# Kernel optimization log

Hardware: AMD Instinct MI355X
Metric: run time of the kernel (lower is better)

Reference implementation:

```python
import jax, jax.numpy as jnp
import numpy as np

B, S, D, H, DFF, N_LAYERS, BLK = 4, 1024, 1024, 16, 4096, 4, 64
DH = D // H
LN_EPS = 1e-5


def setup_inputs() -> dict:
    key = jax.random.key(0)
    ks = jax.random.split(key, 13)
    s = 0.02
    L = N_LAYERS
    return {
        "x": jax.random.normal(ks[0], (B, S, D), jnp.float32),
        "in_proj_w": jax.random.normal(ks[1], (L, 3 * D, D), jnp.float32) * s,
        "in_proj_b": jnp.zeros((L, 3 * D), jnp.float32),
        "out_w": jax.random.normal(ks[2], (L, D, D), jnp.float32) * s,
        "out_b": jnp.zeros((L, D), jnp.float32),
        "ln1_w": jnp.ones((L, D), jnp.float32),
        "ln1_b": jnp.zeros((L, D), jnp.float32),
        "lin1_w": jax.random.normal(ks[3], (L, DFF, D), jnp.float32) * s,
        "lin1_b": jnp.zeros((L, DFF), jnp.float32),
        "lin2_w": jax.random.normal(ks[4], (L, D, DFF), jnp.float32) * s,
        "lin2_b": jnp.zeros((L, D), jnp.float32),
        "ln2_w": jnp.ones((L, D), jnp.float32),
        "ln2_b": jnp.zeros((L, D), jnp.float32),
    }


def _layer_norm(x, w, b):
    mu = jnp.mean(x, axis=-1, keepdims=True)
    var = jnp.mean(jnp.square(x - mu), axis=-1, keepdims=True)
    return (x - mu) * jax.lax.rsqrt(var + LN_EPS) * w + b


def _forward(x, in_proj_w, in_proj_b, out_w, out_b, ln1_w, ln1_b,
             lin1_w, lin1_b, lin2_w, lin2_b, ln2_w, ln2_b):
    # block-causal additive bias: token may attend to current and previous blocks
    blk = jnp.arange(S) // BLK
    bias = jnp.where(blk[:, None] >= blk[None, :], 0.0, -jnp.inf)  # [S,S]
    scale = 1.0 / np.sqrt(DH).astype(np.float32)

    for l in range(N_LAYERS):
        # --- self-attention (post-norm, PyTorch TransformerEncoderLayer default) ---
        qkv = x @ in_proj_w[l].T + in_proj_b[l]            # [B,S,3D]
        q, k, v = jnp.split(qkv, 3, axis=-1)
        q = q.reshape(B, S, H, DH).transpose(0, 2, 1, 3)   # [B,H,S,DH]
        k = k.reshape(B, S, H, DH).transpose(0, 2, 1, 3)
        v = v.reshape(B, S, H, DH).transpose(0, 2, 1, 3)
        scores = jnp.einsum('bhqd,bhkd->bhqk', q, k) * scale + bias
        attn = jax.nn.softmax(scores, axis=-1)
        o = jnp.einsum('bhqk,bhkd->bhqd', attn, v)
        o = o.transpose(0, 2, 1, 3).reshape(B, S, D)
        o = o @ out_w[l].T + out_b[l]
        x = _layer_norm(x + o, ln1_w[l], ln1_b[l])
        # --- feed-forward (relu) ---
        h = jax.nn.relu(x @ lin1_w[l].T + lin1_b[l]) @ lin2_w[l].T + lin2_b[l]
        x = _layer_norm(x + h, ln2_w[l], ln2_b[l])
    return x


def reference(x, in_proj_w, in_proj_b, out_w, out_b, ln1_w, ln1_b,
              lin1_w, lin1_b, lin2_w, lin2_b, ln2_w, ln2_b):
    return _forward(x, in_proj_w, in_proj_b, out_w, out_b, ln1_w, ln1_b,
                    lin1_w, lin1_b, lin2_w, lin2_b, ln2_w, ln2_b)
```

## Files before the change

### kernel.cpp

```cpp
#include <hip/hip_runtime.h>
#include <stdint.h>

typedef __bf16 bf16;
typedef __bf16 bf16x8 __attribute__((ext_vector_type(8)));
typedef __bf16 bf16x4 __attribute__((ext_vector_type(4)));
typedef float  f32x4  __attribute__((ext_vector_type(4)));

#define B_   4
#define S_   1024
#define D_   1024
#define H_   16
#define DH_  64
#define DFF_ 4096
#define NL_  4
#define M_   (B_*S_)

__device__ __forceinline__ void async_copy16(const void* g, void* l) {
  __builtin_amdgcn_global_load_lds(
      (const __attribute__((address_space(1))) char*)(uintptr_t)g,
      (__attribute__((address_space(3))) char*)(uintptr_t)l,
      16, 0, 0);
}

template<int RELU, int MODE, int QKV, int BK>
__global__ __launch_bounds__(256) void gemm_bt_kernel(
    const bf16* __restrict__ A,
    const bf16* __restrict__ W,
    const float* __restrict__ bias,
    float* __restrict__ Cf,
    bf16*  __restrict__ Cb,
    bf16*  __restrict__ VtOut,
    int N, int Ktot, int Kc, int gx, int PN, int PM, int bpk)
{
  constexpr int NI = (BK == 64) ? 4 : 2;
  __shared__ bf16 As[2][128*BK];
  __shared__ bf16 Bs[2][128*BK];

  const int tid  = threadIdx.x;
  const int wave = tid >> 6;
  const int lane = tid & 63;
  const int wr = wave >> 1, wc = wave & 1;
  const int q4  = lane >> 4;
  const int l15 = lane & 15;

  const int Lg  = blockIdx.x;
  const int kz  = Lg / bpk;
  const int L   = Lg % bpk;
  const int xcd = L & 7;
  const int s   = L >> 3;
  const int Gn  = gx / PN;
  const int bn = ((xcd % Gn)*PN + (s % PN)) << 7;
  const int bm = ((xcd / Gn)*PM + (s / PN)) << 7;
  const int kstart = kz * Kc;

  const bf16* agp[NI]; const bf16* wgp[NI];
  int ldsb[NI];
  if constexpr (BK == 64) {
    const int r_loc = lane >> 3, c8 = lane & 7;
#pragma unroll
    for (int j = 0; j < NI; ++j) {
      const int rr = wave*32 + j*8 + r_loc;
      const int ko = ((c8 ^ (rr & 7)) << 3);
      agp[j] = A + (size_t)(bm + rr)*Ktot + kstart + ko;
      wgp[j] = W + (size_t)(bn + rr)*Ktot + kstart + ko;
      ldsb[j] = (wave*32 + j*8) * 64;
    }
  } else {
    const int r_loc = lane >> 2, c4 = lane & 3;
#pragma unroll
    for (int j = 0; j < NI; ++j) {
      const int rr = wave*32 + j*16 + r_loc;
      const int ko = ((c4 ^ ((rr >> 1) & 3)) << 3);
      agp[j] = A + (size_t)(bm + rr)*Ktot + kstart + ko;
      wgp[j] = W + (size_t)(bn + rr)*Ktot + kstart + ko;
      ldsb[j] = (wave*32 + j*16) * 32;
    }
  }

  f32x4 acc[4][4] = {};
  const int steps = Kc / BK;

  auto stage = [&](int buf) {
#pragma unroll
    for (int j = 0; j < NI; ++j) {
      async_copy16(agp[j], &As[buf][ldsb[j]]);
      async_copy16(wgp[j], &Bs[buf][ldsb[j]]);
      agp[j] += BK; wgp[j] += BK;
    }
  };

  const int sl32 = (l15 >> 1) & 3;
  const int sl64 = l15 & 7;

  auto compute = [&](int buf) {
    if constexpr (BK == 64) {
#pragma unroll
      for (int kk = 0; kk < 2; ++kk) {
        const int ch = (((kk << 2) | q4) ^ sl64) << 3;
        bf16x8 af[4], bfr[4];
#pragma unroll
        for (int rf = 0; rf < 4; ++rf)
          af[rf] = *(const bf16x8*)&As[buf][(wr*64 + rf*16 + l15)*64 + ch];
#pragma unroll
        for (int cf = 0; cf < 4; ++cf)
          bfr[cf] = *(const bf16x8*)&Bs[buf][(wc*64 + cf*16 + l15)*64 + ch];
#pragma unroll
        for (int rf = 0; rf < 4; ++rf)
#pragma unroll
          for (int cf = 0; cf < 4; ++cf)
            acc[rf][cf] = __builtin_amdgcn_mfma_f32_16x16x32_bf16(
                af[rf], bfr[cf], acc[rf][cf], 0, 0, 0);
      }
    } else {
      const int ch = (q4 ^ sl32) << 3;
      bf16x8 af[4], bfr[4];
#pragma unroll
      for (int rf = 0; rf < 4; ++rf)
        af[rf] = *(const bf16x8*)&As[buf][(wr*64 + rf*16 + l15)*32 + ch];
#pragma unroll
      for (int cf = 0; cf < 4; ++cf)
        bfr[cf] = *(const bf16x8*)&Bs[buf][(wc*64 + cf*16 + l15)*32 + ch];
#pragma unroll
      for (int rf = 0; rf < 4; ++rf)
#pragma unroll
        for (int cf = 0; cf < 4; ++cf)
          acc[rf][cf] = __builtin_amdgcn_mfma_f32_16x16x32_bf16(
              af[rf], bfr[cf], acc[rf][cf], 0, 0, 0);
    }
  };

  stage(0);
  __syncthreads();
  for (int k = 0; k < steps; ++k) {
    const int cur = k & 1;
    if (k + 1 < steps) stage(cur ^ 1);
    compute(cur);
    __syncthreads();
  }

  if (QKV && bn >= 2*D_) {
#pragma unroll
    for (int r = 0; r < 4; ++r) {
      const int row0 = bm + wr*64 + r*16 + q4*4;
      const int bidx = row0 >> 10, s0 = row0 & 1023;
#pragma unroll
      for (int c = 0; c < 4; ++c) {
        const int col  = bn + wc*64 + c*16 + l15;
        const int dcol = col - 2*D_;
        const int hh = dcol >> 6, dd = dcol & 63;
        const float bv = bias[col];
        bf16x4 pk;
#pragma unroll
        for (int i = 0; i < 4; ++i) pk[i] = (bf16)(acc[r][c][i] + bv);
        *(bf16x4*)&VtOut[((size_t)((bidx*H_ + hh)*64 + dd))*S_ + s0] = pk;
      }
    }
  } else if (MODE == 2) {
    float* Cfz = Cf + (size_t)kz * ((size_t)M_ * N);
#pragma unroll
    for (int r = 0; r < 4; ++r) {
      const int row0 = bm + wr*64 + r*16 + q4*4;
#pragma unroll
      for (int c = 0; c < 4; ++c) {
        const int col = bn + wc*64 + c*16 + l15;
#pragma unroll
        for (int i = 0; i < 4; ++i)
          Cfz[(size_t)(row0 + i)*N + col] = acc[r][c][i];
      }
    }
  } else {
#pragma unroll
    for (int r = 0; r < 4; ++r) {
      const int row0 = bm + wr*64 + r*16 + q4*4;
#pragma unroll
      for (int c = 0; c < 4; ++c) {
        const int col = bn + wc*64 + c*16 + l15;
        const float bv = bias[col];
#pragma unroll
        for (int i = 0; i < 4; ++i) {
          float v = acc[r][c][i] + bv;
          if (RELU) v = fmaxf(v, 0.f);
          Cb[(size_t)(row0 + i)*N + col] = (bf16)v;
        }
      }
    }
  }
}

#define LP 72
__global__ __launch_bounds__(256) void attn_kernel(
    const bf16* __restrict__ qkv,
    const bf16* __restrict__ vt,
    bf16* __restrict__ out)
{
  const int L    = blockIdx.x;
  const int xcd  = L & 7, slot = L >> 3;
  const int qb   = slot & 15;
  const int bh   = xcd*8 + (slot >> 4);
  const int b    = bh >> 4, h = bh & 15;
  const int tid  = threadIdx.x;
  const int wave = tid >> 6, lane = tid & 63;
  const int q4 = lane >> 4, l15 = lane & 15;
  const int r_loc = lane >> 3, c8 = lane & 7;

  __shared__ bf16 Qs[64*64];
  __shared__ bf16 Ks[2][64*64];
  __shared__ bf16 Vs[2][64*64];
  __shared__ bf16 Ps[4][16*LP];

  const size_t RS = 3*(size_t)D_;
  const bf16* qg = qkv + (size_t)(b*S_ + qb*64)*RS + h*64;
  const bf16* kg = qkv + (size_t)(b*S_)*RS + D_ + h*64;
  const bf16* vg = vt + (size_t)bh*64*S_;

#pragma unroll
  for (int j = 0; j < 2; ++j) {
    const int rr = wave*16 + j*8 + r_loc;
    const int ko = ((c8 ^ (rr & 7)) << 3);
    async_copy16(qg + (size_t)rr*RS + ko, &Qs[(wave*16 + j*8)*64]);
  }

#define STAGE_KV(KT, BUF)                                              \
  {                                                                    \
    _Pragma("unroll")                                                  \
    for (int j = 0; j < 2; ++j) {                                      \
      const int rr = wave*16 + j*8 + r_loc;                            \
      const int ko = ((c8 ^ (rr & 7)) << 3);                           \
      async_copy16(kg + (size_t)((KT)*64 + rr)*RS + ko,                \
                   &Ks[BUF][(wave*16 + j*8)*64]);                      \
      async_copy16(vg + (size_t)rr*S_ + (KT)*64 + ko,                  \
                   &Vs[BUF][(wave*16 + j*8)*64]);                      \
    }                                                                  \
  }

  f32x4 o_acc[4] = {};
  float m_i[4], l_i[4];
#pragma unroll
  for (int i = 0; i < 4; ++i) { m_i[i] = -1e30f; l_i[i] = 0.f; }
  const float scale = 0.125f;

  STAGE_KV(0, 0)
  __syncthreads();

  for (int kt = 0; kt <= qb; ++kt) {
    const int cur = kt & 1;
    if (kt < qb) {
      if (cur) STAGE_KV(kt+1, 0) else STAGE_KV(kt+1, 1)
    }

    f32x4 sc[4] = {};
#pragma unroll
    for (int kk = 0; kk < 2; ++kk) {
      const int go = ((((kk << 2) | q4)) ^ (l15 & 7)) << 3;
      bf16x8 aq = *(const bf16x8*)&Qs[(wave*16 + l15)*64 + go];
#pragma unroll
      for (int c = 0; c < 4; ++c) {
        bf16x8 bk = *(const bf16x8*)&Ks[cur][(c*16 + l15)*64 + go];
        sc[c] = __builtin_amdgcn_mfma_f32_16x16x32_bf16(aq, bk, sc[c], 0, 0, 0);
      }
    }
#pragma unroll
    for (int c = 0; c < 4; ++c)
#pragma unroll
      for (int i = 0; i < 4; ++i) sc[c][i] *= scale;

#pragma unroll
    for (int i = 0; i < 4; ++i) {
      float mx = -1e30f;
#pragma unroll
      for (int c = 0; c < 4; ++c) mx = fmaxf(mx, sc[c][i]);
#pragma unroll
      for (int off = 1; off < 16; off <<= 1) mx = fmaxf(mx, __shfl_xor(mx, off, 64));
      float m_new = fmaxf(m_i[i], mx);
      float alpha = __expf(m_i[i] - m_new);
      float rowsum = 0.f;
#pragma unroll
      for (int c = 0; c < 4; ++c) {
        float p = __expf(sc[c][i] - m_new);
        Ps[wave][(q4*4 + i)*LP + c*16 + l15] = (bf16)p;
        rowsum += p;
      }
#pragma unroll
      for (int off = 1; off < 16; off <<= 1) rowsum += __shfl_xor(rowsum, off, 64);
      l_i[i] = l_i[i]*alpha + rowsum;
      m_i[i] = m_new;
#pragma unroll
      for (int c = 0; c < 4; ++c) o_acc[c][i] *= alpha;
    }

#pragma unroll
    for (int kk = 0; kk < 2; ++kk) {
      bf16x8 ap = *(const bf16x8*)&Ps[wave][l15*LP + kk*32 + q4*8];
#pragma unroll
      for (int c = 0; c < 4; ++c) {
        const int go = ((((kk << 2) | q4)) ^ (l15 & 7)) << 3;
        bf16x8 bv = *(const bf16x8*)&Vs[cur][(c*16 + l15)*64 + go];
        o_acc[c] = __builtin_amdgcn_mfma_f32_16x16x32_bf16(ap, bv, o_acc[c], 0, 0, 0);
      }
    }
    __syncthreads();
  }
#undef STAGE_KV

  bf16* obase = out + ((size_t)(b*S_ + qb*64 + wave*16))*D_ + h*64;
#pragma unroll
  for (int i = 0; i < 4; ++i) {
    float inv = 1.f / l_i[i];
#pragma unroll
    for (int c = 0; c < 4; ++c)
      obase[(size_t)(q4*4 + i)*D_ + c*16 + l15] = (bf16)(o_acc[c][i]*inv);
  }
}

__global__ __launch_bounds__(256) void add_ln_kernel(
    const float* __restrict__ xin, const float* __restrict__ parts,
    const float* __restrict__ ybias,
    const float* __restrict__ w, const float* __restrict__ bta,
    float* __restrict__ xout, bf16* __restrict__ xbf,
    float* __restrict__ extra)
{
  const int row = blockIdx.x;
  const int tid = threadIdx.x;
  const size_t base = (size_t)row * D_;
  const size_t PS = (size_t)M_ * D_;
  float v[4], sm = 0.f, ss = 0.f;
#pragma unroll
  for (int j = 0; j < 4; ++j) {
    int idx = tid + j*256;
    float y = ybias[idx] + parts[base + idx] + parts[PS + base + idx];
    v[j] = xin[base + idx] + y;
    sm += v[j]; ss += v[j]*v[j];
  }
#pragma unroll
  for (int off = 1; off < 64; off <<= 1) {
    sm += __shfl_xor(sm, off, 64);
    ss += __shfl_xor(ss, off, 64);
  }
  __shared__ float red[8];
  const int wave = tid >> 6, lane = tid & 63;
  if (lane == 0) { red[wave] = sm; red[4 + wave] = ss; }
  __syncthreads();
  sm = red[0] + red[1] + red[2] + red[3];
  ss = red[4] + red[5] + red[6] + red[7];
  const float mean = sm * (1.f/D_);
  const float var  = ss * (1.f/D_) - mean*mean;
  const float rstd = rsqrtf(var + 1e-5f);
#pragma unroll
  for (int j = 0; j < 4; ++j) {
    int idx = tid + j*256;
    float o = (v[j] - mean)*rstd*w[idx] + bta[idx];
    xout[base + idx] = o;
    xbf[base + idx]  = (bf16)o;
    if (extra) extra[base + idx] = o;
  }
}

__global__ __launch_bounds__(256) void conv_kernel(
    const float4* __restrict__ src, bf16x4* __restrict__ dst, int n4)
{
  int i = blockIdx.x*blockDim.x + threadIdx.x;
  const int stride = gridDim.x*blockDim.x;
  for (; i < n4; i += stride) {
    float4 f = src[i];
    bf16x4 o;
    o[0] = (bf16)f.x; o[1] = (bf16)f.y; o[2] = (bf16)f.z; o[3] = (bf16)f.w;
    dst[i] = o;
  }
}

__global__ __launch_bounds__(256) void init_x_kernel(
    const float4* __restrict__ src, float4* __restrict__ xf,
    bf16x4* __restrict__ xb, int n4)
{
  int i = blockIdx.x*blockDim.x + threadIdx.x;
  const int stride = gridDim.x*blockDim.x;
  for (; i < n4; i += stride) {
    float4 f = src[i];
    xf[i] = f;
    bf16x4 o;
    o[0] = (bf16)f.x; o[1] = (bf16)f.y; o[2] = (bf16)f.z; o[3] = (bf16)f.w;
    xb[i] = o;
  }
}

extern "C" void kernel_launch(void* const* d_in, const int* in_sizes, int n_in,
                              void* d_out, int out_size, void* d_ws, size_t ws_size,
                              hipStream_t stream) {
  const float* x    = (const float*)d_in[0];
  const float* inw  = (const float*)d_in[1];
  const float* inb  = (const float*)d_in[2];
  const float* outw = (const float*)d_in[3];
  const float* outb = (const float*)d_in[4];
  const float* ln1w = (const float*)d_in[5];
  const float* ln1b = (const float*)d_in[6];
  const float* l1w  = (const float*)d_in[7];
  const float* l1b  = (const float*)d_in[8];
  const float* l2w  = (const float*)d_in[9];
  const float* l2b  = (const float*)d_in[10];
  const float* ln2w = (const float*)d_in[11];
  const float* ln2b = (const float*)d_in[12];

  char* ws = (char*)d_ws;
  size_t off = 0;
  auto take = [&](size_t bytes) {
    char* p = ws + off;
    off = (off + bytes + 255) & ~(size_t)255;
    return p;
  };
  bf16*  w_in_bf  = (bf16*) take((size_t)NL_*3*D_*D_*2);
  bf16*  w_out_bf = (bf16*) take((size_t)NL_*D_*D_*2);
  bf16*  w_l1_bf  = (bf16*) take((size_t)NL_*DFF_*D_*2);
  bf16*  w_l2_bf  = (bf16*) take((size_t)NL_*D_*DFF_*2);
  float* x_f      = (float*)take((size_t)M_*D_*4);
  bf16*  x_b      = (bf16*) take((size_t)M_*D_*2);
  bf16*  qkv_b    = (bf16*) take((size_t)M_*3*D_*2);
  bf16*  vt_b     = (bf16*) take((size_t)B_*H_*DH_*S_*2);
  bf16*  at_b     = (bf16*) take((size_t)M_*D_*2);
  bf16*  h_b      = (bf16*) take((size_t)M_*DFF_*2);
  float* parts    = (float*)take((size_t)2*M_*D_*4);
  (void)ws_size; (void)in_sizes; (void)n_in;

  auto conv = [&](const float* s, bf16* d, size_t n) {
    int n4 = (int)(n >> 2);
    int grid = (n4 + 255) / 256; if (grid > 4096) grid = 4096;
    conv_kernel<<<grid, 256, 0, stream>>>((const float4*)s, (bf16x4*)d, n4);
  };
  conv(inw,  w_in_bf,  (size_t)NL_*3*D_*D_);
  conv(outw, w_out_bf, (size_t)NL_*D_*D_);
  conv(l1w,  w_l1_bf,  (size_t)NL_*DFF_*D_);
  conv(l2w,  w_l2_bf,  (size_t)NL_*D_*DFF_);
  init_x_kernel<<<4096, 256, 0, stream>>>((const float4*)x, (float4*)x_f,
                                          (bf16x4*)x_b, (int)((size_t)M_*D_ >> 2));

  for (int l = 0; l < NL_; ++l) {
    gemm_bt_kernel<0,1,1,32><<<768, 256, 0, stream>>>(
        x_b, w_in_bf + (size_t)l*3*D_*D_, inb + (size_t)l*3*D_,
        nullptr, qkv_b, vt_b, 3*D_, D_, D_, 24, 12, 8, 768);
    attn_kernel<<<1024, 256, 0, stream>>>(qkv_b, vt_b, at_b);
    gemm_bt_kernel<0,2,0,64><<<512, 256, 0, stream>>>(
        at_b, w_out_bf + (size_t)l*D_*D_, nullptr,
        parts, nullptr, nullptr, D_, D_, D_/2, 8, 4, 8, 256);
    add_ln_kernel<<<M_, 256, 0, stream>>>(
        x_f, parts, outb + (size_t)l*D_,
        ln1w + (size_t)l*D_, ln1b + (size_t)l*D_, x_f, x_b, nullptr);
    gemm_bt_kernel<1,1,0,32><<<1024, 256, 0, stream>>>(
        x_b, w_l1_bf + (size_t)l*DFF_*D_, l1b + (size_t)l*DFF_,
        nullptr, h_b, nullptr, DFF_, D_, D_, 32, 16, 8, 1024);
    gemm_bt_kernel<0,2,0,64><<<512, 256, 0, stream>>>(
        h_b, w_l2_bf + (size_t)l*D_*DFF_, nullptr,
        parts, nullptr, nullptr, D_, DFF_, DFF_/2, 8, 4, 8, 256);
    add_ln_kernel<<<M_, 256, 0, stream>>>(
        x_f, parts, l2b + (size_t)l*D_,
        ln2w + (size_t)l*D_, ln2b + (size_t)l*D_, x_f, x_b,
        (l == NL_-1) ? (float*)d_out : nullptr);
  }
}
```

Measured before the change: 1.112 ms.

## Add 256x256-tile 8-wave GEMM kernel for QKV, FFN1 and FFN2

Introduces a new GEMM kernel with 256x256 output tiles, 512 threads (8 waves), a double-buffered LDS pipeline with async global-to-LDS copies, explicit vmcnt waits and barriers, and s_setprio around the MFMA blocks. It replaces the 128x128 kernel for the QKV projection and both FFN GEMMs. FFN2 switches to a 4-way split-K, so the partial buffer grows and the add+layernorm kernel is templated on the number of partials. The larger tiles raise operand reuse per block, at the cost of fewer blocks (192-256) on a 256-CU part, more workspace, and more partial-sum traffic for FFN2.

```diff
diff --git a/kernel.cpp b/kernel.cpp
--- a/kernel.cpp
+++ b/kernel.cpp
@@ -22,14 +22,164 @@
       16, 0, 0);
 }
 
-template<int RELU, int MODE, int QKV, int BK>
-__global__ __launch_bounds__(256) void gemm_bt_kernel(
+#define WAITV4 asm volatile("s_waitcnt vmcnt(4)" ::: "memory")
+#define WAITV0 asm volatile("s_waitcnt vmcnt(0)" ::: "memory")
+#define BAR()  { asm volatile("" ::: "memory"); __builtin_amdgcn_s_barrier(); \
+                 asm volatile("" ::: "memory"); }
+
+template<int RELU, int MODE, int QKV>
+__global__ __launch_bounds__(512, 2) void gemm256_kernel(
     const bf16* __restrict__ A,
     const bf16* __restrict__ W,
     const float* __restrict__ bias,
     float* __restrict__ Cf,
     bf16*  __restrict__ Cb,
     bf16*  __restrict__ VtOut,
+    int N, int Ktot, int Kc, int gx, int PN, int PM, int bpk)
+{
+  __shared__ __align__(16) bf16 As[2][2][256*32];
+  __shared__ __align__(16) bf16 Bs[2][2][256*32];
+
+  const int tid  = threadIdx.x;
+  const int wave = tid >> 6;
+  const int lane = tid & 63;
+  const int wr = wave >> 2, wc = wave & 3;
+  const int q4  = lane >> 4;
+  const int l15 = lane & 15;
+
+  const int Lg  = blockIdx.x;
+  const int kz  = Lg / bpk;
+  const int L   = Lg % bpk;
+  const int xcd = L & 7;
+  const int s   = L >> 3;
+  const int Gn  = gx / PN;
+  const int bn = ((xcd % Gn)*PN + (s % PN)) << 8;
+  const int bm = ((xcd / Gn)*PM + (s / PN)) << 8;
+  const int kstart = kz * Kc;
+
+  const int r_loc = lane >> 2, c4 = lane & 3;
+  const int sko = (c4 ^ ((r_loc >> 1) & 3)) << 3;
+  const bf16* agp[2]; const bf16* wgp[2];
+#pragma unroll
+  for (int j = 0; j < 2; ++j) {
+    const int rr = j*128 + wave*16 + r_loc;
+    agp[j] = A + (size_t)(bm + rr)*Ktot + kstart + sko;
+    wgp[j] = W + (size_t)(bn + rr)*Ktot + kstart + sko;
+  }
+
+  auto stageA = [&](int buf, int kk, int koff) {
+#pragma unroll
+    for (int j = 0; j < 2; ++j)
+      async_copy16(agp[j] + koff + kk*32, &As[buf][kk][(j*128 + wave*16)*32]);
+  };
+  auto stageB = [&](int buf, int kk, int koff) {
+#pragma unroll
+    for (int j = 0; j < 2; ++j)
+      async_copy16(wgp[j] + koff + kk*32, &Bs[buf][kk][(j*128 + wave*16)*32]);
+  };
+
+  const int ch = ((q4 ^ ((l15 >> 1) & 3)) << 3);
+
+  f32x4 acc[8][4] = {};
+  const int steps = Kc / 64;
+
+  stageA(0, 0, 0); stageB(0, 0, 0); stageA(0, 1, 0); stageB(0, 1, 0);
+  WAITV4;
+  BAR();
+
+  int koff = 64;
+  for (int t = 0; t < steps; ++t) {
+    const int c = t & 1;
+    const bool pf = (t + 1 < steps);
+    bf16x8 bfr[4];
+#pragma unroll
+    for (int p = 0; p < 4; ++p) {
+      const int kk = p >> 1, rh = p & 1;
+      if (rh == 0) {
+#pragma unroll
+        for (int cf = 0; cf < 4; ++cf)
+          bfr[cf] = *(const bf16x8*)&Bs[c][kk][(wc*64 + cf*16 + l15)*32 + ch];
+      }
+      bf16x8 af[4];
+#pragma unroll
+      for (int r4 = 0; r4 < 4; ++r4)
+        af[r4] = *(const bf16x8*)&As[c][kk][(wr*128 + (rh*4 + r4)*16 + l15)*32 + ch];
+      if (pf) {
+        if      (p == 0) stageA(c ^ 1, 0, koff);
+        else if (p == 1) stageB(c ^ 1, 0, koff);
+        else if (p == 2) stageA(c ^ 1, 1, koff);
+        else             stageB(c ^ 1, 1, koff);
+      }
+      BAR();
+      __builtin_amdgcn_s_setprio(1);
+#pragma unroll
+      for (int r4 = 0; r4 < 4; ++r4)
+#pragma unroll
+        for (int cf = 0; cf < 4; ++cf)
+          acc[rh*4 + r4][cf] = __builtin_amdgcn_mfma_f32_16x16x32_bf16(
+              af[r4], bfr[cf], acc[rh*4 + r4][cf], 0, 0, 0);
+      __builtin_amdgcn_s_setprio(0);
+      if (p == 1) { if (pf) { WAITV4; } else { WAITV0; } }
+      if (p == 3) { if (pf) { WAITV4; } }
+      BAR();
+    }
+    koff += 64;
+  }
+
+  if (QKV && bn >= 2*D_) {
+#pragma unroll
+    for (int r = 0; r < 8; ++r) {
+      const int row0 = bm + wr*128 + r*16 + q4*4;
+      const int bidx = row0 >> 10, s0 = row0 & 1023;
+#pragma unroll
+      for (int cf = 0; cf < 4; ++cf) {
+        const int col  = bn + wc*64 + cf*16 + l15;
+        const int dcol = col - 2*D_;
+        const int hh = dcol >> 6, dd = dcol & 63;
+        const float bv = bias[col];
+        bf16x4 pk;
+#pragma unroll
+        for (int i = 0; i < 4; ++i) pk[i] = (bf16)(acc[r][cf][i] + bv);
+        *(bf16x4*)&VtOut[((size_t)((bidx*H_ + hh)*64 + dd))*S_ + s0] = pk;
+      }
+    }
+  } else if (MODE == 2) {
+    float* Cfz = Cf + (size_t)kz * ((size_t)M_ * N);
+#pragma unroll
+    for (int r = 0; r < 8; ++r) {
+      const int row0 = bm + wr*128 + r*16 + q4*4;
+#pragma unroll
+      for (int cf = 0; cf < 4; ++cf) {
+        const int col = bn + wc*64 + cf*16 + l15;
+#pragma unroll
+        for (int i = 0; i < 4; ++i)
+          Cfz[(size_t)(row0 + i)*N + col] = acc[r][cf][i];
+      }
+    }
+  } else {
+#pragma unroll
+    for (int r = 0; r < 8; ++r) {
+      const int row0 = bm + wr*128 + r*16 + q4*4;
+#pragma unroll
+      for (int cf = 0; cf < 4; ++cf) {
+        const int col = bn + wc*64 + cf*16 + l15;
+        const float bv = bias[col];
+#pragma unroll
+        for (int i = 0; i < 4; ++i) {
+          float v = acc[r][cf][i] + bv;
+          if (RELU) v = fmaxf(v, 0.f);
+          Cb[(size_t)(row0 + i)*N + col] = (bf16)v;
+        }
+      }
+    }
+  }
+}
+
+template<int RELU, int MODE, int QKV, int BK>
+__global__ __launch_bounds__(256) void gemm_bt_kernel(
+    const bf16* __restrict__ A, const bf16* __restrict__ W,
+    const float* __restrict__ bias, float* __restrict__ Cf,
+    bf16*  __restrict__ Cb, bf16*  __restrict__ VtOut,
     int N, int Ktot, int Kc, int gx, int PN, int PM, int bpk)
 {
   constexpr int NI = (BK == 64) ? 4 : 2;
@@ -312,6 +462,7 @@
   }
 }
 
+template<int NP>
 __global__ __launch_bounds__(256) void add_ln_kernel(
     const float* __restrict__ xin, const float* __restrict__ parts,
     const float* __restrict__ ybias,
@@ -327,7 +478,9 @@
 #pragma unroll
   for (int j = 0; j < 4; ++j) {
     int idx = tid + j*256;
-    float y = ybias[idx] + parts[base + idx] + parts[PS + base + idx];
+    float y = ybias[idx];
+#pragma unroll
+    for (int pz = 0; pz < NP; ++pz) y += parts[(size_t)pz*PS + base + idx];
     v[j] = xin[base + idx] + y;
     sm += v[j]; ss += v[j]*v[j];
   }
@@ -417,7 +570,7 @@
   bf16*  vt_b     = (bf16*) take((size_t)B_*H_*DH_*S_*2);
   bf16*  at_b     = (bf16*) take((size_t)M_*D_*2);
   bf16*  h_b      = (bf16*) take((size_t)M_*DFF_*2);
-  float* parts    = (float*)take((size_t)2*M_*D_*4);
+  float* parts    = (float*)take((size_t)4*M_*D_*4);
   (void)ws_size; (void)in_sizes; (void)n_in;
 
   auto conv = [&](const float* s, bf16* d, size_t n) {
@@ -433,23 +586,23 @@
                                           (bf16x4*)x_b, (int)((size_t)M_*D_ >> 2));
 
   for (int l = 0; l < NL_; ++l) {
-    gemm_bt_kernel<0,1,1,32><<<768, 256, 0, stream>>>(
+    gemm256_kernel<0,1,1><<<192, 512, 0, stream>>>(
         x_b, w_in_bf + (size_t)l*3*D_*D_, inb + (size_t)l*3*D_,
-        nullptr, qkv_b, vt_b, 3*D_, D_, D_, 24, 12, 8, 768);
+        nullptr, qkv_b, vt_b, 3*D_, D_, D_, 12, 3, 8, 192);
     attn_kernel<<<1024, 256, 0, stream>>>(qkv_b, vt_b, at_b);
     gemm_bt_kernel<0,2,0,64><<<512, 256, 0, stream>>>(
         at_b, w_out_bf + (size_t)l*D_*D_, nullptr,
         parts, nullptr, nullptr, D_, D_, D_/2, 8, 4, 8, 256);
-    add_ln_kernel<<<M_, 256, 0, stream>>>(
+    add_ln_kernel<2><<<M_, 256, 0, stream>>>(
         x_f, parts, outb + (size_t)l*D_,
         ln1w + (size_t)l*D_, ln1b + (size_t)l*D_, x_f, x_b, nullptr);
-    gemm_bt_kernel<1,1,0,32><<<1024, 256, 0, stream>>>(
+    gemm256_kernel<1,1,0><<<256, 512, 0, stream>>>(
         x_b, w_l1_bf + (size_t)l*DFF_*D_, l1b + (size_t)l*DFF_,
-        nullptr, h_b, nullptr, DFF_, D_, D_, 32, 16, 8, 1024);
-    gemm_bt_kernel<0,2,0,64><<<512, 256, 0, stream>>>(
+        nullptr, h_b, nullptr, DFF_, D_, D_, 16, 4, 8, 256);
+    gemm256_kernel<0,2,0><<<256, 512, 0, stream>>>(
         h_b, w_l2_bf + (size_t)l*D_*DFF_, nullptr,
-        parts, nullptr, nullptr, D_, DFF_, DFF_/2, 8, 4, 8, 256);
-    add_ln_kernel<<<M_, 256, 0, stream>>>(
+        parts, nullptr, nullptr, D_, DFF_, DFF_/4, 4, 1, 8, 64);
+    add_ln_kernel<4><<<M_, 256, 0, stream>>>(
         x_f, parts, l2b + (size_t)l*D_,
         ln2w + (size_t)l*D_, ln2b + (size_t)l*D_, x_f, x_b,
         (l == NL_-1) ? (float*)d_out : nullptr);
```

New measurement: 1.106 ms. No clear change (-0.5%).
